# Performance work log

Measured on AMD Instinct MI355X. Metric: run time of the kernel, lower is better.

Reference implementation:

```python
import jax, jax.numpy as jnp
import numpy as np

N, L, S, D, H = 4, 8192, 8192, 256, 8
DH = D // H  # 32
EPS_ATTN = 1e-6
EPS_LN = 1e-5


def setup_inputs() -> dict:
    key = jax.random.key(0)
    ks = jax.random.split(key, 8)
    w = lambda k, sh: jax.random.normal(k, sh, jnp.float32) * 0.02
    return {
        "x": jax.random.normal(ks[0], (N, L, D), jnp.float32),
        "source": jax.random.normal(ks[1], (N, S, D), jnp.float32),
        "Wq": w(ks[2], (D, D)),
        "Wk": w(ks[3], (D, D)),
        "Wv": w(ks[4], (D, D)),
        "Wm": w(ks[5], (D, D)),
        "W1": w(ks[6], (2 * D, 2 * D)),
        "W2": w(ks[7], (2 * D, D)),
        "g1": jnp.ones((D,), jnp.float32),
        "b1": jnp.zeros((D,), jnp.float32),
        "g2": jnp.ones((D,), jnp.float32),
        "b2": jnp.zeros((D,), jnp.float32),
    }


def _layernorm(x, g, b):
    m = jnp.mean(x, axis=-1, keepdims=True)
    v = jnp.var(x, axis=-1, keepdims=True)
    return (x - m) * jax.lax.rsqrt(v + EPS_LN) * g + b


def reference(x, source, Wq, Wk, Wv, Wm, W1, W2, g1, b1, g2, b2):
    bs = x.shape[0]
    # QKV projections (bias=False), split heads -> [N, L/S, H, DH]
    q = (x @ Wq).reshape(bs, -1, H, DH)
    k = (source @ Wk).reshape(bs, -1, H, DH)
    v = (source @ Wv).reshape(bs, -1, H, DH)
    # elu+1 feature map (linear attention, LoFTR-style)
    Q = jax.nn.elu(q) + 1.0
    K = jax.nn.elu(k) + 1.0
    v_len = v.shape[1]
    vals = v / v_len
    KV = jnp.einsum("nshd,nshv->nhdv", K, vals)  # [N, H, DH, DH]
    Z = 1.0 / (jnp.einsum("nlhd,nhd->nlh", Q, K.sum(axis=1)) + EPS_ATTN)
    msg = jnp.einsum("nlhd,nhdv,nlh->nlhv", Q, KV, Z) * v_len  # [N, L, H, DH]
    # merge heads + LN
    msg = msg.reshape(bs, -1, H * DH) @ Wm
    msg = _layernorm(msg, g1, b1)
    # concat-MLP with LeakyReLU(0.1)
    h = jnp.concatenate([x, msg], axis=2) @ W1
    h = jnp.where(h >= 0, h, 0.1 * h)
    msg = h @ W2
    msg = _layernorm(msg, g2, b2)
    return x + msg
```

## Files before the change

### kernel.cpp

```cpp
#include <hip/hip_runtime.h>

typedef __bf16 bf16;
typedef __bf16 bf16x4 __attribute__((ext_vector_type(4)));
typedef __bf16 bf16x8 __attribute__((ext_vector_type(8)));
typedef float f32x4 __attribute__((ext_vector_type(4)));

#define BM 128
#define BN 128
#define BK 64

__device__ __forceinline__ float apply_epi(float v, int epi) {
  if (epi == 1) return v > 0.f ? v + 1.f : __expf(v);
  if (epi == 2) return v >= 0.f ? v : 0.1f * v;
  return v;
}

__device__ __forceinline__ void g2l16(const bf16* gp, bf16* lp) {
  __builtin_amdgcn_global_load_lds(
      (const __attribute__((address_space(1))) void*)gp,
      (__attribute__((address_space(3))) void*)lp, 16, 0, 0);
}

__global__ void detect_kernel(const unsigned* g1raw, int* flag) {
  if (threadIdx.x == 0 && blockIdx.x == 0)
    *flag = (g1raw[0] == 0x3F800000u) ? 1 : 0;
}

struct TransArgs {
  const void* src[6];
  bf16* dst[6];
  int R[6], C[6], t0[6];
};

__global__ __launch_bounds__(256) void prep_kernel(
    const void* __restrict__ xin, const void* __restrict__ sin,
    bf16* __restrict__ bx, bf16* __restrict__ bs,
    TransArgs ta, const int* flagp) {
  const bool f32 = (*flagp != 0);
  if (blockIdx.x < 8192) {
    const void* s;
    bf16* d;
    size_t i;
    if (blockIdx.x < 4096) {
      s = xin; d = bx; i = (size_t)blockIdx.x * 2048 + threadIdx.x * 8;
    } else {
      s = sin; d = bs; i = (size_t)(blockIdx.x - 4096) * 2048 + threadIdx.x * 8;
    }
    if (f32) {
      f32x4 lo = *(const f32x4*)((const float*)s + i);
      f32x4 hi = *(const f32x4*)((const float*)s + i + 4);
      bf16x8 t;
      t[0] = (bf16)lo[0]; t[1] = (bf16)lo[1]; t[2] = (bf16)lo[2]; t[3] = (bf16)lo[3];
      t[4] = (bf16)hi[0]; t[5] = (bf16)hi[1]; t[6] = (bf16)hi[2]; t[7] = (bf16)hi[3];
      *(bf16x8*)(d + i) = t;
    } else {
      *(bf16x8*)(d + i) = *(const bf16x8*)((const bf16*)s + i);
    }
    return;
  }
  __shared__ bf16 tile[32][33];
  int bid = blockIdx.x - 8192;
  int si = 0;
#pragma unroll
  for (int i = 1; i < 6; ++i)
    if (bid >= ta.t0[i]) si = i;
  const void* srcv = ta.src[si];
  bf16* dst = ta.dst[si];
  int R = ta.R[si], Cc = ta.C[si];
  int lt = bid - ta.t0[si];
  int tpr = Cc >> 5;
  int tr = lt / tpr, tc = lt % tpr;
  int tx = threadIdx.x & 31, ty0 = threadIdx.x >> 5;
#pragma unroll
  for (int i = 0; i < 4; ++i) {
    int ty = ty0 + i * 8;
    size_t idx = (size_t)(tr * 32 + ty) * Cc + tc * 32 + tx;
    tile[ty][tx] = f32 ? (bf16)((const float*)srcv)[idx] : ((const bf16*)srcv)[idx];
  }
  __syncthreads();
#pragma unroll
  for (int i = 0; i < 4; ++i) {
    int ty = ty0 + i * 8;
    dst[(size_t)(tc * 32 + ty) * R + tr * 32 + tx] = tile[tx][ty];
  }
}

__global__ __launch_bounds__(256) void gemm_rt(
    const bf16* __restrict__ A, const bf16* __restrict__ A2, int ldA,
    const bf16* __restrict__ Bt, bf16* __restrict__ C, int Nn, int Kk, int epi,
    bf16* __restrict__ C2, int epi2, int split) {
  __shared__ bf16 As[BM * BK];
  __shared__ bf16 Bs[BN * BK];
  const int tid = threadIdx.x;
  const int m0 = blockIdx.x * BM;
  const int n0 = blockIdx.y * BN;
  const int wave = tid >> 6, lane = tid & 63;
  const int wm = (wave & 1) * 64, wn = (wave >> 1) * 64;
  const int q = lane >> 4, mr = lane & 15;

  f32x4 acc[4][4];
#pragma unroll
  for (int i = 0; i < 4; ++i)
#pragma unroll
    for (int j = 0; j < 4; ++j) acc[i][j] = (f32x4){0.f, 0.f, 0.f, 0.f};

  const int kTiles = Kk / BK;
  for (int kt = 0; kt < kTiles; ++kt) {
    int kk = kt * BK;
    const bf16* Ab = A;
    int kcol = kk;
    if (A2 && kk >= 256) { Ab = A2; kcol = kk - 256; }
    __syncthreads();
#pragma unroll
    for (int it = 0; it < 4; ++it) {
      int id = it * 256 + tid;
      int rr = id >> 3, pp = id & 7, gg = pp ^ (rr & 7);
      g2l16(Ab + (size_t)(m0 + rr) * ldA + kcol + gg * 8, &As[id * 8]);
    }
#pragma unroll
    for (int it = 0; it < 4; ++it) {
      int id = it * 256 + tid;
      int rr = id >> 3, pp = id & 7, gg = pp ^ (rr & 7);
      g2l16(Bt + (size_t)(n0 + rr) * Kk + kk + gg * 8, &Bs[id * 8]);
    }
    __syncthreads();
#pragma unroll
    for (int ks = 0; ks < 2; ++ks) {
      bf16x8 af[4], bfv[4];
#pragma unroll
      for (int mi = 0; mi < 4; ++mi) {
        int rrow = wm + mi * 16 + mr;
        af[mi] = *(const bf16x8*)&As[rrow * BK + ((ks * 4 + q) ^ (rrow & 7)) * 8];
      }
#pragma unroll
      for (int ni = 0; ni < 4; ++ni) {
        int rrow = wn + ni * 16 + mr;
        bfv[ni] = *(const bf16x8*)&Bs[rrow * BK + ((ks * 4 + q) ^ (rrow & 7)) * 8];
      }
#pragma unroll
      for (int mi = 0; mi < 4; ++mi)
#pragma unroll
        for (int ni = 0; ni < 4; ++ni)
          acc[mi][ni] = __builtin_amdgcn_mfma_f32_16x16x32_bf16(af[mi], bfv[ni], acc[mi][ni], 0, 0, 0);
    }
  }

  bf16* Cw = C;
  int nbase = n0, ep = epi;
  if (C2 && n0 >= split) { Cw = C2; nbase = n0 - split; ep = epi2; }
#pragma unroll
  for (int mi = 0; mi < 4; ++mi)
#pragma unroll
    for (int ni = 0; ni < 4; ++ni)
#pragma unroll
      for (int r4 = 0; r4 < 4; ++r4) {
        int row = m0 + wm + mi * 16 + q * 4 + r4;
        int cn = nbase + wn + ni * 16 + mr;
        float v = apply_epi(acc[mi][ni][r4], ep);
        Cw[(size_t)row * Nn + cn] = (bf16)v;
      }
}

#define KVCH 256
__global__ __launch_bounds__(256) void kv_kernel(
    const bf16* __restrict__ Kf, const bf16* __restrict__ V,
    float* __restrict__ partial, float* __restrict__ pk) {
  __shared__ bf16 Ks[KVCH][32];
  __shared__ bf16 Vs[KVCH][32];
  const int cb = blockIdx.x, h = blockIdx.y, n = blockIdx.z;
  const int tid = threadIdx.x;
  const int wave = tid >> 6, lane = tid & 63;
  const int d0 = (lane & 7) * 4, dv0 = (lane >> 3) * 4;
  const int s0 = cb * KVCH;
#pragma unroll
  for (int rd = 0; rd < 4; ++rd) {
    int rr = rd * 64 + (tid >> 2), pp = tid & 3;
    size_t g = ((size_t)(n * 8192 + s0 + rr)) * 256 + h * 32 + pp * 8;
    *(bf16x8*)&Ks[rr][pp * 8] = *(const bf16x8*)(Kf + g);
    *(bf16x8*)&Vs[rr][pp * 8] = *(const bf16x8*)(V + g);
  }
  __syncthreads();
  float acc[4][4] = {};
  float ks4[4] = {};
#pragma unroll 4
  for (int si = 0; si < 64; ++si) {
    int s = wave * 64 + si;
    bf16x4 k4 = *(const bf16x4*)&Ks[s][d0];
    bf16x4 v4 = *(const bf16x4*)&Vs[s][dv0];
    float kf[4] = {(float)k4[0], (float)k4[1], (float)k4[2], (float)k4[3]};
    float vf[4] = {(float)v4[0], (float)v4[1], (float)v4[2], (float)v4[3]};
#pragma unroll
    for (int vi = 0; vi < 4; ++vi)
#pragma unroll
      for (int di = 0; di < 4; ++di) acc[vi][di] = fmaf(vf[vi], kf[di], acc[vi][di]);
#pragma unroll
    for (int di = 0; di < 4; ++di) ks4[di] += kf[di];
  }
  __syncthreads();
  float* red = (float*)&Ks[0][0];
  float* ksr = (float*)&Vs[0][0];
#pragma unroll
  for (int vi = 0; vi < 4; ++vi)
#pragma unroll
    for (int di = 0; di < 4; ++di)
      red[wave * 1024 + (dv0 + vi) * 32 + d0 + di] = acc[vi][di];
  if (dv0 == 0) {
#pragma unroll
    for (int di = 0; di < 4; ++di) ksr[wave * 32 + d0 + di] = ks4[di];
  }
  __syncthreads();
  const size_t slot = (size_t)(n * 8 + h) * 32 + cb;
  f32x4 s4 = {0.f, 0.f, 0.f, 0.f};
#pragma unroll
  for (int w = 0; w < 4; ++w) s4 += *(const f32x4*)&red[w * 1024 + tid * 4];
  *(f32x4*)&partial[slot * 1024 + tid * 4] = s4;
  if (tid < 32) {
    float ss = 0.f;
#pragma unroll
    for (int w = 0; w < 4; ++w) ss += ksr[w * 32 + tid];
    pk[slot * 32 + tid] = ss;
  }
}

__global__ __launch_bounds__(256) void kv_reduce(
    const float* __restrict__ partial, const float* __restrict__ pk,
    float* __restrict__ kv_acc, float* __restrict__ ksum) {
  const int b = blockIdx.x;
  const int t = threadIdx.x;
  f32x4 s4 = {0.f, 0.f, 0.f, 0.f};
  for (int c = 0; c < 32; ++c)
    s4 += *(const f32x4*)&partial[((size_t)b * 32 + c) * 1024 + t * 4];
  *(f32x4*)&kv_acc[(size_t)b * 1024 + t * 4] = s4;
  if (t < 32) {
    float ss = 0.f;
    for (int c = 0; c < 32; ++c) ss += pk[((size_t)b * 32 + c) * 32 + t];
    ksum[(size_t)b * 32 + t] = ss;
  }
}

__global__ __launch_bounds__(256) void msg_kernel(
    const bf16* __restrict__ Q, const float* __restrict__ kv_acc,
    const float* __restrict__ ksum, bf16* __restrict__ msg) {
  __shared__ bf16 kvt[8][32][32];
  __shared__ float ksl[8][32];
  __shared__ float zl[8][128];
  int tid = threadIdx.x;
  int row0 = blockIdx.x * 128;
  int n = row0 >> 13;
  const float* kvb = kv_acc + (size_t)n * 8192;
  for (int i = tid; i < 8192; i += 256) ((bf16*)kvt)[i] = (bf16)kvb[i];
  ((float*)ksl)[tid] = ksum[(size_t)n * 256 + tid];
  __syncthreads();
  int r = tid & 127, hg = tid >> 7;
  const bf16* qrow = Q + (size_t)(row0 + r) * 256;
#pragma unroll
  for (int hh = 0; hh < 4; ++hh) {
    int h = hg * 4 + hh;
    float dot = 0.f;
#pragma unroll
    for (int d = 0; d < 32; ++d) dot = fmaf((float)qrow[h * 32 + d], ksl[h][d], dot);
    zl[h][r] = 1.f / (dot + 1e-6f);
  }
  __syncthreads();
  int wave = tid >> 6, lane = tid & 63, q = lane >> 4, mr = lane & 15;
  f32x4 zero = {0.f, 0.f, 0.f, 0.f};
  for (int h = 0; h < 8; ++h) {
    bf16x8 b0 = *(const bf16x8*)&kvt[h][mr][q * 8];
    bf16x8 b1 = *(const bf16x8*)&kvt[h][16 + mr][q * 8];
#pragma unroll
    for (int mi = 0; mi < 2; ++mi) {
      int arow = wave * 32 + mi * 16 + mr;
      bf16x8 a = *(const bf16x8*)(Q + (size_t)(row0 + arow) * 256 + h * 32 + q * 8);
      f32x4 c0 = __builtin_amdgcn_mfma_f32_16x16x32_bf16(a, b0, zero, 0, 0, 0);
      f32x4 c1 = __builtin_amdgcn_mfma_f32_16x16x32_bf16(a, b1, zero, 0, 0, 0);
#pragma unroll
      for (int r4 = 0; r4 < 4; ++r4) {
        int orow = wave * 32 + mi * 16 + q * 4 + r4;
        float z = zl[h][orow];
        size_t ob = (size_t)(row0 + orow) * 256 + h * 32;
        msg[ob + mr] = (bf16)(c0[r4] * z);
        msg[ob + 16 + mr] = (bf16)(c1[r4] * z);
      }
    }
  }
}

__global__ __launch_bounds__(256) void ln_kernel(
    const bf16* __restrict__ in, const void* __restrict__ g, const void* __restrict__ b,
    const void* __restrict__ resid, void* __restrict__ outp,
    const int* flagp, int ioDual) {
  const bool gbF32 = (*flagp != 0);
  const bool ioF32 = ioDual && gbF32;
  int wave = threadIdx.x >> 6, lane = threadIdx.x & 63;
  size_t row = (size_t)blockIdx.x * 4 + wave;
  int c = lane * 4;
  bf16x4 v = *(const bf16x4*)(in + row * 256 + c);
  float x0 = (float)v[0], x1 = (float)v[1], x2 = (float)v[2], x3 = (float)v[3];
  float s = x0 + x1 + x2 + x3;
  float sq = x0 * x0 + x1 * x1 + x2 * x2 + x3 * x3;
#pragma unroll
  for (int o = 32; o > 0; o >>= 1) {
    s += __shfl_xor(s, o);
    sq += __shfl_xor(sq, o);
  }
  float mean = s * (1.f / 256.f);
  float var = sq * (1.f / 256.f) - mean * mean;
  float rstd = rsqrtf(var + 1e-5f);
  float g0, g1v, g2v, g3, b0, b1v, b2v, b3;
  if (gbF32) {
    f32x4 gv = *(const f32x4*)((const float*)g + c);
    f32x4 bv = *(const f32x4*)((const float*)b + c);
    g0 = gv[0]; g1v = gv[1]; g2v = gv[2]; g3 = gv[3];
    b0 = bv[0]; b1v = bv[1]; b2v = bv[2]; b3 = bv[3];
  } else {
    bf16x4 gv = *(const bf16x4*)((const bf16*)g + c);
    bf16x4 bv = *(const bf16x4*)((const bf16*)b + c);
    g0 = (float)gv[0]; g1v = (float)gv[1]; g2v = (float)gv[2]; g3 = (float)gv[3];
    b0 = (float)bv[0]; b1v = (float)bv[1]; b2v = (float)bv[2]; b3 = (float)bv[3];
  }
  float y0 = (x0 - mean) * rstd * g0 + b0;
  float y1 = (x1 - mean) * rstd * g1v + b1v;
  float y2 = (x2 - mean) * rstd * g2v + b2v;
  float y3 = (x3 - mean) * rstd * g3 + b3;
  if (resid) {
    if (ioF32) {
      f32x4 rv = *(const f32x4*)((const float*)resid + row * 256 + c);
      y0 += rv[0]; y1 += rv[1]; y2 += rv[2]; y3 += rv[3];
    } else {
      bf16x4 rv = *(const bf16x4*)((const bf16*)resid + row * 256 + c);
      y0 += (float)rv[0]; y1 += (float)rv[1]; y2 += (float)rv[2]; y3 += (float)rv[3];
    }
  }
  if (ioF32) {
    f32x4 o4 = {y0, y1, y2, y3};
    *(f32x4*)((float*)outp + row * 256 + c) = o4;
  } else {
    bf16x4 o4;
    o4[0] = (bf16)y0; o4[1] = (bf16)y1; o4[2] = (bf16)y2; o4[3] = (bf16)y3;
    *(bf16x4*)((bf16*)outp + row * 256 + c) = o4;
  }
}

extern "C" void kernel_launch(void* const* d_in, const int* in_sizes, int n_in,
                              void* d_out, int out_size, void* d_ws, size_t ws_size,
                              hipStream_t stream) {
  const void* x   = d_in[0];
  const void* src = d_in[1];
  const void* Wq  = d_in[2];
  const void* Wk  = d_in[3];
  const void* Wv  = d_in[4];
  const void* Wm  = d_in[5];
  const void* W1  = d_in[6];
  const void* W2  = d_in[7];
  const void* g1  = d_in[8];
  const void* b1  = d_in[9];
  const void* g2  = d_in[10];
  const void* b2  = d_in[11];

  char* ws = (char*)d_ws;
  bf16* bufA = (bf16*)(ws);
  bf16* bufB = (bf16*)(ws + ((size_t)16 << 20));
  bf16* bufC = (bf16*)(ws + ((size_t)32 << 20));
  bf16* WqT  = (bf16*)(ws + ((size_t)48 << 20));
  bf16* WkvT = WqT + 65536;
  bf16* WmT  = WkvT + 131072;
  bf16* W1T  = WmT + 65536;
  bf16* W2T  = W1T + 262144;
  float* kv_acc = (float*)(ws + ((size_t)50 << 20));
  float* ksum = kv_acc + 32768;
  int* flagp = (int*)(ws + ((size_t)50 << 20) + 160 * 1024);
  float* partial = (float*)(ws + ((size_t)51 << 20));
  float* pk = (float*)(ws + ((size_t)55 << 20));
  bf16* bufX = (bf16*)d_out;
  bf16* bufS = bufX + 8388608;

  detect_kernel<<<dim3(1), dim3(64), 0, stream>>>((const unsigned*)g1, flagp);

  TransArgs ta;
  ta.src[0] = Wq; ta.src[1] = Wk; ta.src[2] = Wv; ta.src[3] = Wm; ta.src[4] = W1; ta.src[5] = W2;
  ta.dst[0] = WqT; ta.dst[1] = WkvT; ta.dst[2] = WkvT + 65536; ta.dst[3] = WmT; ta.dst[4] = W1T; ta.dst[5] = W2T;
  ta.R[0] = 256; ta.R[1] = 256; ta.R[2] = 256; ta.R[3] = 256; ta.R[4] = 512; ta.R[5] = 512;
  ta.C[0] = 256; ta.C[1] = 256; ta.C[2] = 256; ta.C[3] = 256; ta.C[4] = 512; ta.C[5] = 256;
  ta.t0[0] = 0; ta.t0[1] = 64; ta.t0[2] = 128; ta.t0[3] = 192; ta.t0[4] = 256; ta.t0[5] = 512;
  prep_kernel<<<dim3(8832), dim3(256), 0, stream>>>(x, src, bufX, bufS, ta, flagp);

  gemm_rt<<<dim3(256, 2), dim3(256), 0, stream>>>(bufX, nullptr, 256, WqT, bufA, 256, 256, 1,
                                                  nullptr, 0, 0);
  gemm_rt<<<dim3(256, 4), dim3(256), 0, stream>>>(bufS, nullptr, 256, WkvT, bufB, 256, 256, 1,
                                                  bufC, 0, 256);

  kv_kernel<<<dim3(32, 8, 4), dim3(256), 0, stream>>>(bufB, bufC, partial, pk);
  kv_reduce<<<dim3(32), dim3(256), 0, stream>>>(partial, pk, kv_acc, ksum);

  msg_kernel<<<dim3(256), dim3(256), 0, stream>>>(bufA, kv_acc, ksum, bufB);

  gemm_rt<<<dim3(256, 2), dim3(256), 0, stream>>>(bufB, nullptr, 256, WmT, bufA, 256, 256, 0,
                                                  nullptr, 0, 0);

  ln_kernel<<<dim3(8192), dim3(256), 0, stream>>>(bufA, g1, b1, nullptr, bufC, flagp, 0);

  gemm_rt<<<dim3(256, 4), dim3(256), 0, stream>>>(bufX, bufC, 256, W1T, bufA, 512, 512, 2,
                                                  nullptr, 0, 0);

  gemm_rt<<<dim3(256, 2), dim3(256), 0, stream>>>(bufA, nullptr, 512, W2T, bufC, 256, 512, 0,
                                                  nullptr, 0, 0);

  ln_kernel<<<dim3(8192), dim3(256), 0, stream>>>(bufC, g2, b2, x, d_out, flagp, 1);
}
```

Measured before the change: 286.4 us.

## Write K/V projections transposed and compute KV outer products with MFMA

```diff
diff --git a/kernel.cpp b/kernel.cpp
--- a/kernel.cpp
+++ b/kernel.cpp
@@ -88,9 +88,10 @@
 __global__ __launch_bounds__(256) void gemm_rt(
     const bf16* __restrict__ A, const bf16* __restrict__ A2, int ldA,
     const bf16* __restrict__ Bt, bf16* __restrict__ C, int Nn, int Kk, int epi,
-    bf16* __restrict__ C2, int epi2, int split) {
-  __shared__ bf16 As[BM * BK];
-  __shared__ bf16 Bs[BN * BK];
+    bf16* __restrict__ C2, int epi2, int split, int transC) {
+  __shared__ bf16 SH[BM * BK + BN * BK];
+  bf16* As = SH;
+  bf16* Bs = SH + BM * BK;
   const int tid = threadIdx.x;
   const int m0 = blockIdx.x * BM;
   const int n0 = blockIdx.y * BN;
@@ -114,35 +115,60 @@
 #pragma unroll
     for (int it = 0; it < 4; ++it) {
       int id = it * 256 + tid;
-      int rr = id >> 3, pp = id & 7, gg = pp ^ (rr & 7);
-      g2l16(Ab + (size_t)(m0 + rr) * ldA + kcol + gg * 8, &As[id * 8]);
+      int rr = id >> 3, pp = id & 7;
+      g2l16(Ab + (size_t)(m0 + rr) * ldA + kcol + pp * 8, &As[id * 8]);
     }
 #pragma unroll
     for (int it = 0; it < 4; ++it) {
       int id = it * 256 + tid;
-      int rr = id >> 3, pp = id & 7, gg = pp ^ (rr & 7);
-      g2l16(Bt + (size_t)(n0 + rr) * Kk + kk + gg * 8, &Bs[id * 8]);
+      int rr = id >> 3, pp = id & 7;
+      g2l16(Bt + (size_t)(n0 + rr) * Kk + kk + pp * 8, &Bs[id * 8]);
     }
     __syncthreads();
 #pragma unroll
     for (int ks = 0; ks < 2; ++ks) {
       bf16x8 af[4], bfv[4];
 #pragma unroll
-      for (int mi = 0; mi < 4; ++mi) {
-        int rrow = wm + mi * 16 + mr;
-        af[mi] = *(const bf16x8*)&As[rrow * BK + ((ks * 4 + q) ^ (rrow & 7)) * 8];
-      }
-#pragma unroll
-      for (int ni = 0; ni < 4; ++ni) {
-        int rrow = wn + ni * 16 + mr;
-        bfv[ni] = *(const bf16x8*)&Bs[rrow * BK + ((ks * 4 + q) ^ (rrow & 7)) * 8];
-      }
+      for (int mi = 0; mi < 4; ++mi)
+        af[mi] = *(const bf16x8*)&As[(wm + mi * 16 + mr) * BK + (ks * 4 + q) * 8];
+#pragma unroll
+      for (int ni = 0; ni < 4; ++ni)
+        bfv[ni] = *(const bf16x8*)&Bs[(wn + ni * 16 + mr) * BK + (ks * 4 + q) * 8];
 #pragma unroll
       for (int mi = 0; mi < 4; ++mi)
 #pragma unroll
         for (int ni = 0; ni < 4; ++ni)
           acc[mi][ni] = __builtin_amdgcn_mfma_f32_16x16x32_bf16(af[mi], bfv[ni], acc[mi][ni], 0, 0, 0);
     }
+  }
+
+  if (transC) {
+    bf16* TC = C;
+    int cb = n0, ep = epi;
+    if (C2 && n0 >= split) { TC = C2; cb = n0 - split; ep = epi2; }
+#pragma unroll
+    for (int p = 0; p < 2; ++p) {
+      __syncthreads();
+      if ((wave >> 1) == p) {
+#pragma unroll
+        for (int mi = 0; mi < 4; ++mi)
+#pragma unroll
+          for (int ni = 0; ni < 4; ++ni)
+#pragma unroll
+            for (int r4 = 0; r4 < 4; ++r4) {
+              int cl = ni * 16 + mr;
+              int sl = wm + mi * 16 + q * 4 + r4;
+              SH[cl * 136 + sl] = (bf16)apply_epi(acc[mi][ni][r4], ep);
+            }
+      }
+      __syncthreads();
+      int row = tid >> 2, c0 = (tid & 3) * 32;
+      size_t gbase = (size_t)(cb + p * 64 + row) * 32768 + m0 + c0;
+#pragma unroll
+      for (int j = 0; j < 4; ++j)
+        *(bf16x8*)(TC + gbase + j * 8) = *(const bf16x8*)&SH[row * 136 + c0 + j * 8];
+    }
+    return;
   }
 
   bf16* Cw = C;
@@ -161,63 +187,61 @@
       }
 }
 
-#define KVCH 256
-__global__ __launch_bounds__(256) void kv_kernel(
-    const bf16* __restrict__ Kf, const bf16* __restrict__ V,
+#define KSK 256
+#define KLD 264
+__global__ __launch_bounds__(256) void kv_mfma(
+    const bf16* __restrict__ Kt, const bf16* __restrict__ Vt,
     float* __restrict__ partial, float* __restrict__ pk) {
-  __shared__ bf16 Ks[KVCH][32];
-  __shared__ bf16 Vs[KVCH][32];
-  const int cb = blockIdx.x, h = blockIdx.y, n = blockIdx.z;
+  __shared__ bf16 As[32 * KLD];
+  __shared__ bf16 Bs[32 * KLD];
+  __shared__ float ksl[32][8];
+  const int sk = blockIdx.x, h = blockIdx.y, n = blockIdx.z;
   const int tid = threadIdx.x;
   const int wave = tid >> 6, lane = tid & 63;
-  const int d0 = (lane & 7) * 4, dv0 = (lane >> 3) * 4;
-  const int s0 = cb * KVCH;
-#pragma unroll
-  for (int rd = 0; rd < 4; ++rd) {
-    int rr = rd * 64 + (tid >> 2), pp = tid & 3;
-    size_t g = ((size_t)(n * 8192 + s0 + rr)) * 256 + h * 32 + pp * 8;
-    *(bf16x8*)&Ks[rr][pp * 8] = *(const bf16x8*)(Kf + g);
-    *(bf16x8*)&Vs[rr][pp * 8] = *(const bf16x8*)(V + g);
+  const int q = lane >> 4, mr = lane & 15;
+  const int mh = wave & 1, nh = wave >> 1;
+  const size_t colBase = (size_t)n * 8192 + (size_t)sk * KSK;
+  const bf16* Ab = Kt + (size_t)(h * 32) * 32768 + colBase;
+  const bf16* Bb = Vt + (size_t)(h * 32) * 32768 + colBase;
+  const int lrow = tid >> 3, lch = (tid & 7) * 32;
+  f32x4 acc = {0.f, 0.f, 0.f, 0.f};
+  float kreg = 0.f;
+  bf16x8 a4[4], b4[4];
+#pragma unroll
+  for (int j = 0; j < 4; ++j) {
+    a4[j] = *(const bf16x8*)(Ab + (size_t)lrow * 32768 + lch + j * 8);
+    b4[j] = *(const bf16x8*)(Bb + (size_t)lrow * 32768 + lch + j * 8);
+  }
+#pragma unroll
+  for (int j = 0; j < 4; ++j) {
+    *(bf16x8*)&As[lrow * KLD + lch + j * 8] = a4[j];
+    *(bf16x8*)&Bs[lrow * KLD + lch + j * 8] = b4[j];
   }
   __syncthreads();
-  float acc[4][4] = {};
-  float ks4[4] = {};
-#pragma unroll 4
-  for (int si = 0; si < 64; ++si) {
-    int s = wave * 64 + si;
-    bf16x4 k4 = *(const bf16x4*)&Ks[s][d0];
-    bf16x4 v4 = *(const bf16x4*)&Vs[s][dv0];
-    float kf[4] = {(float)k4[0], (float)k4[1], (float)k4[2], (float)k4[3]};
-    float vf[4] = {(float)v4[0], (float)v4[1], (float)v4[2], (float)v4[3]};
-#pragma unroll
-    for (int vi = 0; vi < 4; ++vi)
-#pragma unroll
-      for (int di = 0; di < 4; ++di) acc[vi][di] = fmaf(vf[vi], kf[di], acc[vi][di]);
-#pragma unroll
-    for (int di = 0; di < 4; ++di) ks4[di] += kf[di];
-  }
+#pragma unroll
+  for (int kk = 0; kk < KSK; kk += 32) {
+    bf16x8 af = *(const bf16x8*)&As[(mh * 16 + mr) * KLD + kk + q * 8];
+    bf16x8 bf = *(const bf16x8*)&Bs[(nh * 16 + mr) * KLD + kk + q * 8];
+    acc = __builtin_amdgcn_mfma_f32_16x16x32_bf16(af, bf, acc, 0, 0, 0);
+  }
+#pragma unroll
+  for (int j = 0; j < 4; ++j) {
+    bf16x8 kx = *(const bf16x8*)&As[lrow * KLD + lch + j * 8];
+#pragma unroll
+    for (int e = 0; e < 8; ++e) kreg += (float)kx[e];
+  }
+  const size_t slot = (size_t)(n * 8 + h) * 32 + sk;
+#pragma unroll
+  for (int r = 0; r < 4; ++r) {
+    int d = mh * 16 + q * 4 + r, dv = nh * 16 + mr;
+    partial[slot * 1024 + (size_t)dv * 32 + d] = acc[r];
+  }
+  ksl[lrow][tid & 7] = kreg;
   __syncthreads();
-  float* red = (float*)&Ks[0][0];
-  float* ksr = (float*)&Vs[0][0];
-#pragma unroll
-  for (int vi = 0; vi < 4; ++vi)
-#pragma unroll
-    for (int di = 0; di < 4; ++di)
-      red[wave * 1024 + (dv0 + vi) * 32 + d0 + di] = acc[vi][di];
-  if (dv0 == 0) {
-#pragma unroll
-    for (int di = 0; di < 4; ++di) ksr[wave * 32 + d0 + di] = ks4[di];
-  }
-  __syncthreads();
-  const size_t slot = (size_t)(n * 8 + h) * 32 + cb;
-  f32x4 s4 = {0.f, 0.f, 0.f, 0.f};
-#pragma unroll
-  for (int w = 0; w < 4; ++w) s4 += *(const f32x4*)&red[w * 1024 + tid * 4];
-  *(f32x4*)&partial[slot * 1024 + tid * 4] = s4;
   if (tid < 32) {
     float ss = 0.f;
 #pragma unroll
-    for (int w = 0; w < 4; ++w) ss += ksr[w * 32 + tid];
+    for (int e = 0; e < 8; ++e) ss += ksl[tid][e];
     pk[slot * 32 + tid] = ss;
   }
 }
@@ -385,25 +409,25 @@
   prep_kernel<<<dim3(8832), dim3(256), 0, stream>>>(x, src, bufX, bufS, ta, flagp);
 
   gemm_rt<<<dim3(256, 2), dim3(256), 0, stream>>>(bufX, nullptr, 256, WqT, bufA, 256, 256, 1,
-                                                  nullptr, 0, 0);
+                                                  nullptr, 0, 0, 0);
   gemm_rt<<<dim3(256, 4), dim3(256), 0, stream>>>(bufS, nullptr, 256, WkvT, bufB, 256, 256, 1,
-                                                  bufC, 0, 256);
-
-  kv_kernel<<<dim3(32, 8, 4), dim3(256), 0, stream>>>(bufB, bufC, partial, pk);
+                                                  bufC, 0, 256, 1);
+
+  kv_mfma<<<dim3(32, 8, 4), dim3(256), 0, stream>>>(bufB, bufC, partial, pk);
   kv_reduce<<<dim3(32), dim3(256), 0, stream>>>(partial, pk, kv_acc, ksum);
 
   msg_kernel<<<dim3(256), dim3(256), 0, stream>>>(bufA, kv_acc, ksum, bufB);
 
   gemm_rt<<<dim3(256, 2), dim3(256), 0, stream>>>(bufB, nullptr, 256, WmT, bufA, 256, 256, 0,
-                                                  nullptr, 0, 0);
+                                                  nullptr, 0, 0, 0);
 
   ln_kernel<<<dim3(8192), dim3(256), 0, stream>>>(bufA, g1, b1, nullptr, bufC, flagp, 0);
 
   gemm_rt<<<dim3(256, 4), dim3(256), 0, stream>>>(bufX, bufC, 256, W1T, bufA, 512, 512, 2,
-                                                  nullptr, 0, 0);
+                                                  nullptr, 0, 0, 0);
 
   gemm_rt<<<dim3(256, 2), dim3(256), 0, stream>>>(bufA, nullptr, 512, W2T, bufC, 256, 512, 0,
-                                                  nullptr, 0, 0);
+                                                  nullptr, 0, 0, 0);
 
   ln_kernel<<<dim3(8192), dim3(256), 0, stream>>>(bufC, g2, b2, x, d_out, flagp, 1);
 }
```

After: 295.7 us. 3.3% more time.
